# Kernel optimization log

Measured on AMD Instinct MI355X. Metric: run time of the kernel, lower is better.

Reference implementation:

```python
import jax, jax.numpy as jnp
import numpy as np


def setup_inputs() -> dict:
    key = jax.random.key(0)
    k1, k2 = jax.random.split(key)
    N, M, D = 16384, 16384, 3
    target_pc = jax.random.normal(k1, (N, D), dtype=jnp.float32)
    output_pc = jax.random.normal(k2, (M, D), dtype=jnp.float32)
    return {"target_pc": target_pc, "output_pc": output_pc}


def _min_dist_sum(a, b):
    # sum over rows of min_j ||a_i - b_j||, via the norm-expansion trick
    sq_a = jnp.sum(a * a, axis=1, keepdims=True)          # [N,1]
    sq_b = jnp.sum(b * b, axis=1, keepdims=True).T        # [1,M]
    sq_dst = sq_a - 2.0 * (a @ b.T) + sq_b                # [N,M]
    dist = jnp.sqrt(jnp.maximum(sq_dst, 0.0))
    return jnp.sum(jnp.min(dist, axis=1))


def reference(target_pc, output_pc):
    loss_a_to_b = _min_dist_sum(output_pc, target_pc)
    loss_b_to_a = _min_dist_sum(target_pc, output_pc)
    return (loss_a_to_b + loss_b_to_a) / 1000.0
```

## Files before the change

### kernel.cpp

```cpp
#include <hip/hip_runtime.h>
#include <cfloat>

#define NPTS 16384
#define C_CHUNKS 64
#define CHUNK (NPTS / C_CHUNKS)
#define NA 8
#define NBLOCKS (2 * C_CHUNKS * NPTS / (256 * NA))

__global__ __launch_bounds__(256) void chamfer_min_kernel(
    const float* __restrict__ target, const float* __restrict__ output,
    int* __restrict__ minsq)
{
    __shared__ float4 bs[CHUNK];

    const int dir = blockIdx.z;
    const float* __restrict__ A = dir ? target : output;
    const float* __restrict__ B = dir ? output : target;

    const int j0 = blockIdx.y * CHUNK;
    {
        int k = threadIdx.x;
        int j = j0 + k;
        float x = B[3 * j], y = B[3 * j + 1], z = B[3 * j + 2];
        bs[k] = make_float4(-2.f * x, -2.f * y, -2.f * z,
                            fmaf(x, x, fmaf(y, y, z * z)));
    }

    const int i0 = blockIdx.x * (256 * NA) + threadIdx.x;
    float ax[NA], ay[NA], az[NA], sqa[NA], m[NA];
    #pragma unroll
    for (int k = 0; k < NA; ++k) {
        int i = i0 + k * 256;
        ax[k] = A[3 * i]; ay[k] = A[3 * i + 1]; az[k] = A[3 * i + 2];
        sqa[k] = fmaf(ax[k], ax[k], fmaf(ay[k], ay[k], az[k] * az[k]));
        m[k] = FLT_MAX;
    }
    __syncthreads();

    #pragma unroll 4
    for (int j = 0; j < CHUNK; j += 2) {
        float4 p = bs[j];
        float4 q = bs[j + 1];
        #pragma unroll
        for (int k = 0; k < NA; ++k) {
            float s0 = fmaf(ax[k], p.x, fmaf(ay[k], p.y, fmaf(az[k], p.z, p.w)));
            float s1 = fmaf(ax[k], q.x, fmaf(ay[k], q.y, fmaf(az[k], q.z, q.w)));
            m[k] = fminf(m[k], fminf(s0, s1));
        }
    }

    #pragma unroll
    for (int k = 0; k < NA; ++k)
        atomicMin(&minsq[dir * NPTS + i0 + k * 256], __float_as_int(m[k] + sqa[k]));
}

__global__ __launch_bounds__(256) void reduce_kernel(
    const int* __restrict__ minsq, float* __restrict__ out)
{
    float s = 0.f;
    const int4* mv = (const int4*)minsq;
    for (int k = blockIdx.x * 256 + threadIdx.x; k < 2 * NPTS / 4; k += gridDim.x * 256) {
        int4 v = mv[k];
        s += sqrtf(fmaxf(__int_as_float(v.x), 0.f))
           + sqrtf(fmaxf(__int_as_float(v.y), 0.f))
           + sqrtf(fmaxf(__int_as_float(v.z), 0.f))
           + sqrtf(fmaxf(__int_as_float(v.w), 0.f));
    }
    for (int off = 32; off; off >>= 1) s += __shfl_down(s, off, 64);
    __shared__ float partial[4];
    if ((threadIdx.x & 63) == 0) partial[threadIdx.x >> 6] = s;
    __syncthreads();
    if (threadIdx.x == 0)
        atomicAdd(out, (partial[0] + partial[1] + partial[2] + partial[3]) * 0.001f);
}

extern "C" void kernel_launch(void* const* d_in, const int* in_sizes, int n_in,
                              void* d_out, int out_size, void* d_ws, size_t ws_size,
                              hipStream_t stream) {
    const float* target = (const float*)d_in[0];
    const float* output = (const float*)d_in[1];
    float* out = (float*)d_out;
    int* minsq = (int*)d_ws;

    hipMemsetAsync(minsq, 0x7F, 2 * NPTS * sizeof(int), stream);
    hipMemsetAsync(out, 0, sizeof(float), stream);

    chamfer_min_kernel<<<dim3(NPTS / (256 * NA), C_CHUNKS, 2), 256, 0, stream>>>(
        target, output, minsq);
    reduce_kernel<<<32, 256, 0, stream>>>(minsq, out);
}
```

Baseline: 101.1 us.

## Compute pairwise squared distances with bf16 split-precision MFMA instead of FMA loops

Adds a pack kernel that splits coordinates, -2x terms and squared norms into hi/lo bf16 pairs laid out as MFMA fragments. The main kernel then uses 32x32x16 bf16 MFMA to produce full squared-distance tiles and takes running mins on the output, with cross-lane shuffles and atomicMin at the end. The aim is to move the distance arithmetic from scalar FMA onto the matrix units. In exchange it adds an extra kernel launch, a workspace round trip and a min reduction per MFMA output element. The bf16 hi/lo split also loses some precision in the distances.

```diff
diff --git a/kernel.cpp b/kernel.cpp
--- a/kernel.cpp
+++ b/kernel.cpp
@@ -1,57 +1,129 @@
 #include <hip/hip_runtime.h>
+#include <hip/hip_bf16.h>
 #include <cfloat>
 
 #define NPTS 16384
-#define C_CHUNKS 64
-#define CHUNK (NPTS / C_CHUNKS)
-#define NA 8
-#define NBLOCKS (2 * C_CHUNKS * NPTS / (256 * NA))
+#define NTILES 512
+#define R 4
+#define BS 8
+#define CPT (NTILES / BS)
 
-__global__ __launch_bounds__(256) void chamfer_min_kernel(
+typedef short short8  __attribute__((ext_vector_type(8)));
+typedef float f32x16  __attribute__((ext_vector_type(16)));
+
+__device__ inline short bf16s(float x) {
+    __hip_bfloat16 h = __float2bfloat16(x);
+    return *reinterpret_cast<short*>(&h);
+}
+__device__ inline float bf16f(short s) {
+    __hip_bfloat16 h = *reinterpret_cast<__hip_bfloat16*>(&s);
+    return __bfloat162float(h);
+}
+
+__global__ __launch_bounds__(256) void pack_kernel(
     const float* __restrict__ target, const float* __restrict__ output,
+    short8* __restrict__ afrag, short8* __restrict__ bfrag)
+{
+    int t = blockIdx.x * 256 + threadIdx.x;
+    int lane = t & 63;
+    int tile = (t >> 6) & (NTILES - 1);
+    int dir  = t >> 15;
+    const float* __restrict__ A = dir ? target : output;
+    const float* __restrict__ B = dir ? output : target;
+    int p = tile * 32 + (lane & 31);
+    int g = lane >> 5;
+    int idx = (dir * NTILES + tile) * 64 + lane;
+
+    {
+        float x = A[3 * p], y = A[3 * p + 1], z = A[3 * p + 2];
+        short hx = bf16s(x), hy = bf16s(y), hz = bf16s(z);
+        short lx = bf16s(x - bf16f(hx)), ly = bf16s(y - bf16f(hy)), lz = bf16s(z - bf16f(hz));
+        float sq = fmaf(x, x, fmaf(y, y, z * z));
+        short sh = bf16s(sq), sl = bf16s(sq - bf16f(sh));
+        const short one = 0x3F80;
+        short8 loa = { hx, hy, hz, lx, ly, lz, hx, hy };
+        short8 hia = { hz, one, one, sh, sl, 0, 0, 0 };
+        afrag[idx] = g ? hia : loa;
+    }
+    {
+        float x = B[3 * p], y = B[3 * p + 1], z = B[3 * p + 2];
+        float nx = -2.f * x, ny = -2.f * y, nz = -2.f * z;
+        short hx = bf16s(nx), hy = bf16s(ny), hz = bf16s(nz);
+        short lx = bf16s(nx - bf16f(hx)), ly = bf16s(ny - bf16f(hy)), lz = bf16s(nz - bf16f(hz));
+        float sq = fmaf(x, x, fmaf(y, y, z * z));
+        short sh = bf16s(sq), sl = bf16s(sq - bf16f(sh));
+        const short one = 0x3F80;
+        short8 lob = { hx, hy, hz, hx, hy, hz, lx, ly };
+        short8 hib = { lz, sh, sl, one, one, 0, 0, 0 };
+        bfrag[idx] = g ? hib : lob;
+    }
+}
+
+__global__ __launch_bounds__(256) void chamfer_mfma_kernel(
+    const short8* __restrict__ afrag, const short8* __restrict__ bfrag,
     int* __restrict__ minsq)
 {
-    __shared__ float4 bs[CHUNK];
+    const int lane = threadIdx.x & 63;
+    const int wid  = blockIdx.x * 4 + (threadIdx.x >> 6);
+    const int dir  = wid >> 10;
+    const int rem  = wid & 1023;
+    const int ag   = rem >> 3;
+    const int bc   = rem & 7;
 
-    const int dir = blockIdx.z;
-    const float* __restrict__ A = dir ? target : output;
-    const float* __restrict__ B = dir ? output : target;
+    const short8* __restrict__ af = afrag + (size_t)dir * NTILES * 64;
+    const short8* __restrict__ bf = bfrag + (size_t)dir * NTILES * 64;
 
-    const int j0 = blockIdx.y * CHUNK;
-    {
-        int k = threadIdx.x;
-        int j = j0 + k;
-        float x = B[3 * j], y = B[3 * j + 1], z = B[3 * j + 2];
-        bs[k] = make_float4(-2.f * x, -2.f * y, -2.f * z,
-                            fmaf(x, x, fmaf(y, y, z * z)));
-    }
+    short8 a[R];
+    #pragma unroll
+    for (int r = 0; r < R; ++r)
+        a[r] = af[(ag * R + r) * 64 + lane];
 
-    const int i0 = blockIdx.x * (256 * NA) + threadIdx.x;
-    float ax[NA], ay[NA], az[NA], sqa[NA], m[NA];
+    f32x16 m[R];
     #pragma unroll
-    for (int k = 0; k < NA; ++k) {
-        int i = i0 + k * 256;
-        ax[k] = A[3 * i]; ay[k] = A[3 * i + 1]; az[k] = A[3 * i + 2];
-        sqa[k] = fmaf(ax[k], ax[k], fmaf(ay[k], ay[k], az[k] * az[k]));
-        m[k] = FLT_MAX;
-    }
-    __syncthreads();
+    for (int r = 0; r < R; ++r)
+        m[r] = (f32x16)(FLT_MAX);
 
-    #pragma unroll 4
-    for (int j = 0; j < CHUNK; j += 2) {
-        float4 p = bs[j];
-        float4 q = bs[j + 1];
+    const f32x16 zero = (f32x16)(0.0f);
+    const int bt0 = bc * CPT;
+    for (int pp = 0; pp < CPT / 2; ++pp) {
+        short8 b0 = bf[(bt0 + 2 * pp + 0) * 64 + lane];
+        short8 b1 = bf[(bt0 + 2 * pp + 1) * 64 + lane];
         #pragma unroll
-        for (int k = 0; k < NA; ++k) {
-            float s0 = fmaf(ax[k], p.x, fmaf(ay[k], p.y, fmaf(az[k], p.z, p.w)));
-            float s1 = fmaf(ax[k], q.x, fmaf(ay[k], q.y, fmaf(az[k], q.z, q.w)));
-            m[k] = fminf(m[k], fminf(s0, s1));
+        for (int r = 0; r < R; ++r) {
+            f32x16 c0 = __builtin_amdgcn_mfma_f32_32x32x16_bf16(a[r], b0, zero, 0, 0, 0);
+            f32x16 c1 = __builtin_amdgcn_mfma_f32_32x32x16_bf16(a[r], b1, zero, 0, 0, 0);
+            #pragma unroll
+            for (int i = 0; i < 16; ++i)
+                m[r][i] = fminf(m[r][i], fminf(c0[i], c1[i]));
         }
     }
 
     #pragma unroll
-    for (int k = 0; k < NA; ++k)
-        atomicMin(&minsq[dir * NPTS + i0 + k * 256], __float_as_int(m[k] + sqa[k]));
+    for (int r = 0; r < R; ++r) {
+        #pragma unroll
+        for (int i = 0; i < 16; ++i) {
+            float v = m[r][i];
+            v = fminf(v, __shfl_xor(v, 1, 64));
+            v = fminf(v, __shfl_xor(v, 2, 64));
+            v = fminf(v, __shfl_xor(v, 4, 64));
+            v = fminf(v, __shfl_xor(v, 8, 64));
+            v = fminf(v, __shfl_xor(v, 16, 64));
+            m[r][i] = v;
+        }
+    }
+
+    if ((lane & 31) == 0) {
+        const int g = lane >> 5;
+        #pragma unroll
+        for (int r = 0; r < R; ++r) {
+            const int at = ag * R + r;
+            #pragma unroll
+            for (int i = 0; i < 16; ++i) {
+                int row = (i & 3) + 8 * (i >> 2) + 4 * g;
+                atomicMin(&minsq[dir * NPTS + at * 32 + row], __float_as_int(m[r][i]));
+            }
+        }
+    }
 }
 
 __global__ __launch_bounds__(256) void reduce_kernel(
@@ -80,12 +152,15 @@
     const float* target = (const float*)d_in[0];
     const float* output = (const float*)d_in[1];
     float* out = (float*)d_out;
-    int* minsq = (int*)d_ws;
+
+    short8* afrag = (short8*)d_ws;
+    short8* bfrag = afrag + 2 * NTILES * 64;
+    int* minsq = (int*)(bfrag + 2 * NTILES * 64);
 
     hipMemsetAsync(minsq, 0x7F, 2 * NPTS * sizeof(int), stream);
     hipMemsetAsync(out, 0, sizeof(float), stream);
 
-    chamfer_min_kernel<<<dim3(NPTS / (256 * NA), C_CHUNKS, 2), 256, 0, stream>>>(
-        target, output, minsq);
+    pack_kernel<<<2 * NTILES * 64 / 256, 256, 0, stream>>>(target, output, afrag, bfrag);
+    chamfer_mfma_kernel<<<512, 256, 0, stream>>>(afrag, bfrag, minsq);
     reduce_kernel<<<32, 256, 0, stream>>>(minsq, out);
 }
```

Result: no change. 101.0 us (-0.1%).
